# Kernel optimization log

Measured on AMD Instinct MI355X. Metric: run time of the kernel, lower is better.

Reference implementation:

```python
import jax, jax.numpy as jnp
import numpy as np
from math import sqrt

DIM = 1024
RANK = 64
B, T = 4, 4096

def _xavier(key, shape):
    fan_in, fan_out = shape[1], shape[0]
    limit = sqrt(6.0 / (fan_in + fan_out))
    return jax.random.uniform(key, shape, jnp.float32, -limit, limit)

def setup_inputs() -> dict:
    key = jax.random.key(0)
    kx, kq, kk, kv = jax.random.split(key, 4)
    return {
        "x": jax.random.normal(kx, (B, T, DIM), jnp.float32),
        "Q": _xavier(kq, (RANK, DIM)),
        "K": _xavier(kk, (RANK, DIM)),
        "VO": _xavier(kv, (DIM, DIM)),
    }

def reference(x, Q, K, VO):
    dim = x.shape[-1]
    # low-rank projections: [b, t, r]
    xq = jnp.einsum('btd,rd->btr', x, Q)
    xk = jnp.einsum('bue,re->bur', x, K)
    scores = jnp.einsum('btr,bur->btu', xq, xk) / sqrt(dim)
    attn = jax.nn.softmax(scores, axis=2)
    # attn @ x @ VO: contract with VO first (cheap [b,u,d]@[d,e]) then attn
    return jnp.einsum('btu,bue->bte', attn, x @ VO)
```

## Files before the change

kernel.cpp:

```cpp
#include <hip/hip_runtime.h>
#include <hip/hip_bf16.h>

#define BATCH 4
#define SEQ   4096
#define DIM   1024
#define RANK  64

typedef __attribute__((ext_vector_type(8))) short short8;
typedef __attribute__((ext_vector_type(4))) short short4v;
typedef __attribute__((ext_vector_type(4))) float f32x4;

#define MFMA16(a,b,c) __builtin_amdgcn_mfma_f32_16x16x32_bf16((a),(b),(c),0,0,0)

#define XQ_OFF 0
#define XK_OFF (BATCH*SEQ*RANK)
#define VT_OFF (2*BATCH*SEQ*RANK)
#define VT_END (VT_OFF + BATCH*DIM*SEQ)
#define P_OFF  ((size_t)VT_END)
#define P_LEN  ((size_t)BATCH*SEQ*SEQ)

__device__ __forceinline__ short f2b(float f) {
    __hip_bfloat16 h = __float2bfloat16(f);
    short s; __builtin_memcpy(&s, &h, sizeof(short));
    return s;
}
__device__ __forceinline__ float b2f(short s) {
    __hip_bfloat16 h; __builtin_memcpy(&h, &s, sizeof(short));
    return __bfloat162float(h);
}
__device__ __forceinline__ short8 cvt8(const float* __restrict__ p) {
    const float4 f0 = *reinterpret_cast<const float4*>(p);
    const float4 f1 = *reinterpret_cast<const float4*>(p + 4);
    short8 r;
    r[0]=f2b(f0.x); r[1]=f2b(f0.y); r[2]=f2b(f0.z); r[3]=f2b(f0.w);
    r[4]=f2b(f1.x); r[5]=f2b(f1.y); r[6]=f2b(f1.z); r[7]=f2b(f1.w);
    return r;
}
__device__ __forceinline__ void gld16(const short* g, short* l) {
    __builtin_amdgcn_global_load_lds(
        (const __attribute__((address_space(1))) void*)g,
        (__attribute__((address_space(3))) void*)l, 16, 0, 0);
}

__global__ __launch_bounds__(256) void lr_cvt(const float* __restrict__ x,
                                              const float* __restrict__ VO,
                                              const float* __restrict__ Qw,
                                              const float* __restrict__ Kw,
                                              short* __restrict__ xb,
                                              short* __restrict__ VOt,
                                              short* __restrict__ Wb)
{
    const int bid = blockIdx.x, tid = threadIdx.x;
    if (bid < 8192) {
        const size_t base = ((size_t)bid*256 + tid)*8;
        *reinterpret_cast<short8*>(xb + base) = cvt8(x + base);
    } else if (bid < 8448) {
        __shared__ short tr[64*68];
        const int bb = bid - 8192;
        const int dt = bb >> 4, et = bb & 15;
        const int d0 = dt*64, e0 = et*64;
        const int ein = tid & 63, din = tid >> 6;
        #pragma unroll
        for (int j = 0; j < 16; ++j) {
            const int dl = din + j*4;
            tr[ein*68 + dl] = f2b(VO[(size_t)(d0 + dl)*DIM + e0 + ein]);
        }
        __syncthreads();
        const int or_ = tid >> 4, oc = (tid & 15)*4;
        #pragma unroll
        for (int j = 0; j < 4; ++j) {
            const int el = or_ + j*16;
            short4v v;
            v[0]=tr[el*68+oc]; v[1]=tr[el*68+oc+1];
            v[2]=tr[el*68+oc+2]; v[3]=tr[el*68+oc+3];
            *reinterpret_cast<short4v*>(VOt + (size_t)(e0+el)*DIM + d0 + oc) = v;
        }
    } else {
        const int gid = (bid - 8448)*256 + tid;
        const int row = gid >> 7, c8 = (gid & 127)*8;
        const float* src = (row < 64 ? Qw + (size_t)row*DIM
                                     : Kw + (size_t)(row-64)*DIM) + c8;
        *reinterpret_cast<short8*>(Wb + (size_t)row*DIM + c8) = cvt8(src);
    }
}

__global__ __launch_bounds__(256, 4) void lr_proj2(const short* __restrict__ xb,
                                                   const short* __restrict__ Wb,
                                                   short* __restrict__ ws)
{
    __shared__ __align__(16) short As[128*64];
    __shared__ __align__(16) short Bs[128*64];
    const int t0 = blockIdx.x*128;
    const int tid = threadIdx.x, lane = tid & 63, w = tid >> 6;
    const int l15 = lane & 15, g = lane >> 4;
    const int wr = w >> 1, wc = w & 1;
    const short* Ab = xb + (size_t)t0*DIM;
    const short* Bb = Wb;
    const int srow = lane >> 3;
    const int skc  = ((lane & 7) ^ srow)*8;
    const int rx = l15 & 7;

    f32x4 acc[4][4] = {};
    #pragma unroll
    for (int j = 0; j < 4; ++j) {
        const int ch = 4*w + j, row = ch*8 + srow;
        gld16(Ab + (size_t)row*DIM + skc, &As[ch*512]);
        gld16(Bb + (size_t)row*DIM + skc, &Bs[ch*512]);
    }
    for (int kt = 0; kt < 16; ++kt) {
        __syncthreads();
        #pragma unroll
        for (int ks = 0; ks < 2; ++ks) {
            short8 af[4], bfr[4];
            #pragma unroll
            for (int mr = 0; mr < 4; ++mr)
                af[mr] = *reinterpret_cast<const short8*>(
                    &As[(wr*64 + mr*16 + l15)*64 + ((ks*4 + g) ^ rx)*8]);
            #pragma unroll
            for (int ct = 0; ct < 4; ++ct)
                bfr[ct] = *reinterpret_cast<const short8*>(
                    &Bs[(wc*64 + ct*16 + l15)*64 + ((ks*4 + g) ^ rx)*8]);
            #pragma unroll
            for (int mr = 0; mr < 4; ++mr)
                #pragma unroll
                for (int ct = 0; ct < 4; ++ct)
                    acc[mr][ct] = MFMA16(af[mr], bfr[ct], acc[mr][ct]);
        }
        if (kt < 15) {
            __syncthreads();
            const int k0 = (kt + 1)*64;
            #pragma unroll
            for (int j = 0; j < 4; ++j) {
                const int ch = 4*w + j, row = ch*8 + srow;
                gld16(Ab + (size_t)row*DIM + k0 + skc, &As[ch*512]);
                gld16(Bb + (size_t)row*DIM + k0 + skc, &Bs[ch*512]);
            }
        }
    }
    short* xqp = ws + XQ_OFF;
    short* xkp = ws + XK_OFF;
    #pragma unroll
    for (int mr = 0; mr < 4; ++mr)
        #pragma unroll
        for (int rr = 0; rr < 4; ++rr) {
            const int t = t0 + wr*64 + mr*16 + g*4 + rr;
            #pragma unroll
            for (int ct = 0; ct < 4; ++ct) {
                const int r = wc*64 + ct*16 + l15;
                const short v = f2b(acc[mr][ct][rr]);
                if (r < RANK) xqp[(size_t)t*RANK + r] = v;
                else          xkp[(size_t)t*RANK + r - RANK] = v;
            }
        }
}

__global__ __launch_bounds__(512, 2) void lr_vg8(const short* __restrict__ VOt,
                                                 const short* __restrict__ xb,
                                                 short* __restrict__ vT)
{
    extern __shared__ __align__(16) short lds[];
    short* As = lds;
    short* Bs = lds + 32768;
    const int bid = blockIdx.x;
    const int xcd = bid & 7, jb = bid >> 3;
    const int et = xcd >> 1;
    const int bu = (xcd & 1)*32 + jb;
    const int b = bu >> 4, ut = bu & 15;
    const int e0 = et*256, u0 = ut*256;
    const int tid = threadIdx.x, lane = tid & 63, w = tid >> 6;
    const int wr = w >> 2, wc = w & 3;
    const int l15 = lane & 15, g = lane >> 4;
    const int rx = l15 & 7;

    const short* Ab = VOt + (size_t)e0*DIM;
    const short* Bb = xb + ((size_t)(b*SEQ) + u0)*DIM;

    int aA0[2], aA1[2], aB0[2], aB1[2];
    int dA0[2], dA1[2], dB0[2], dB1[2];
    #pragma unroll
    for (int j = 0; j < 2; ++j) {
        const int s = tid + 512*j;
        const int cl = s >> 6, v = s & 63;
        const int vr = v >> 3, vk = ((v & 7) ^ vr)*8;
        const int cA0 = (cl < 8) ? cl : cl + 8;
        const int cA1 = cA0 + 8;
        const int cB0 = ((cl >> 2) << 3) + (cl & 3);
        const int cB1 = cB0 + 4;
        aA0[j] = (cA0*8 + vr)*DIM + vk;  dA0[j] = cA0*512 + v*8;
        aA1[j] = (cA1*8 + vr)*DIM + vk;  dA1[j] = cA1*512 + v*8;
        aB0[j] = (cB0*8 + vr)*DIM + vk;  dB0[j] = cB0*512 + v*8;
        aB1[j] = (cB1*8 + vr)*DIM + vk;  dB1[j] = cB1*512 + v*8;
    }

    f32x4 acc[8][4] = {};
    short8 af[4][2], bf[4][2];

    #pragma unroll
    for (int j = 0; j < 2; ++j) gld16(Ab + aA0[j], &As[dA0[j]]);
    #pragma unroll
    for (int j = 0; j < 2; ++j) gld16(Bb + aB0[j], &Bs[dB0[j]]);
    #pragma unroll
    for (int j = 0; j < 2; ++j) gld16(Bb + aB1[j], &Bs[dB1[j]]);
    #pragma unroll
    for (int j = 0; j < 2; ++j) gld16(Ab + aA1[j], &As[dA1[j]]);
    asm volatile("s_waitcnt vmcnt(4)" ::: "memory");
    __builtin_amdgcn_s_barrier();
    __builtin_amdgcn_sched_barrier(0);

    for (int kt = 0; kt < 15; ++kt) {
        const int buf  = (kt & 1) ? 16384 : 0;
        const int nbuf = 16384 - buf;
        const int kn = (kt + 1)*64;
        const int arow = buf + (wr*128 + l15)*64;
        const int brow = buf + (wc*64 + l15)*64;
        #pragma unroll
        for (int mf = 0; mf < 4; ++mf)
            #pragma unroll
            for (int ks = 0; ks < 2; ++ks)
                af[mf][ks] = *reinterpret_cast<const short8*>(
                    &As[arow + mf*1024 + ((ks*4 + g) ^ rx)*8]);
        #pragma unroll
        for (int nf = 0; nf < 2; ++nf)
            #pragma unroll
            for (int ks = 0; ks < 2; ++ks)
                bf[nf][ks] = *reinterpret_cast<const short8*>(
                    &Bs[brow + nf*1024 + ((ks*4 + g) ^ rx)*8]);
        #pragma unroll
        for (int j = 0; j < 2; ++j) gld16(Ab + aA0[j] + kn, &As[nbuf + dA0[j]]);
        __builtin_amdgcn_s_barrier();
        asm volatile("s_waitcnt lgkmcnt(0)" ::: "memory");
        __builtin_amdgcn_sched_barrier(0);
        __builtin_amdgcn_s_setprio(1);
        #pragma unroll
        for (int mf = 0; mf < 4; ++mf)
            #pragma unroll
            for (int nf = 0; nf < 2; ++nf)
                #pragma unroll
                for (int ks = 0; ks < 2; ++ks)
                    acc[mf][nf] = MFMA16(af[mf][ks], bf[nf][ks], acc[mf][nf]);
        __builtin_amdgcn_s_setprio(0);
        asm volatile("s_waitcnt vmcnt(4)" ::: "memory");
        __builtin_amdgcn_s_barrier();
        __builtin_amdgcn_sched_barrier(0);
        #pragma unroll
        for (int nf = 2; nf < 4; ++nf)
            #pragma unroll
            for (int ks = 0; ks < 2; ++ks)
                bf[nf][ks] = *reinterpret_cast<const short8*>(
                    &Bs[brow + nf*1024 + ((ks*4 + g) ^ rx)*8]);
        #pragma unroll
        for (int j = 0; j < 2; ++j) gld16(Bb + aB0[j] + kn, &Bs[nbuf + dB0[j]]);
        __builtin_amdgcn_s_barrier();
        asm volatile("s_waitcnt lgkmcnt(0)" ::: "memory");
        __builtin_amdgcn_sched_barrier(0);
        __builtin_amdgcn_s_setprio(1);
        #pragma unroll
        for (int mf = 0; mf < 4; ++mf)
            #pragma unroll
            for (int nf = 2; nf < 4; ++nf)
                #pragma unroll
                for (int ks = 0; ks < 2; ++ks)
                    acc[mf][nf] = MFMA16(af[mf][ks], bf[nf][ks], acc[mf][nf]);
        __builtin_amdgcn_s_setprio(0);
        asm volatile("s_waitcnt vmcnt(4)" ::: "memory");
        __builtin_amdgcn_s_barrier();
        __builtin_amdgcn_sched_barrier(0);
        #pragma unroll
        for (int mf = 0; mf < 4; ++mf)
            #pragma unroll
            for (int ks = 0; ks < 2; ++ks)
                af[mf][ks] = *reinterpret_cast<const short8*>(
                    &As[arow + 4096 + mf*1024 + ((ks*4 + g) ^ rx)*8]);
        #pragma unroll
        for (int j = 0; j < 2; ++j) gld16(Bb + aB1[j] + kn, &Bs[nbuf + dB1[j]]);
        __builtin_amdgcn_s_barrier();
        asm volatile("s_waitcnt lgkmcnt(0)" ::: "memory");
        __builtin_amdgcn_sched_barrier(0);
        __builtin_amdgcn_s_setprio(1);
        #pragma unroll
        for (int mf = 0; mf < 4; ++mf)
            #pragma unroll
            for (int nf = 0; nf < 2; ++nf)
                #pragma unroll
                for (int ks = 0; ks < 2; ++ks)
                    acc[mf+4][nf] = MFMA16(af[mf][ks], bf[nf][ks], acc[mf+4][nf]);
        __builtin_amdgcn_s_setprio(0);
        __builtin_amdgcn_s_barrier();
        __builtin_amdgcn_sched_barrier(0);
        #pragma unroll
        for (int j = 0; j < 2; ++j) gld16(Ab + aA1[j] + kn, &As[nbuf + dA1[j]]);
        __builtin_amdgcn_s_setprio(1);
        #pragma unroll
        for (int mf = 0; mf < 4; ++mf)
            #pragma unroll
            for (int nf = 2; nf < 4; ++nf)
                #pragma unroll
                for (int ks = 0; ks < 2; ++ks)
                    acc[mf+4][nf] = MFMA16(af[mf][ks], bf[nf][ks], acc[mf+4][nf]);
        __builtin_amdgcn_s_setprio(0);
        asm volatile("s_waitcnt vmcnt(4)" ::: "memory");
        __builtin_amdgcn_s_barrier();
        __builtin_amdgcn_sched_barrier(0);
    }
    asm volatile("s_waitcnt vmcnt(0)" ::: "memory");
    __builtin_amdgcn_s_barrier();
    __builtin_amdgcn_sched_barrier(0);
    {
        const int arow = 16384 + (wr*128 + l15)*64;
        const int brow = 16384 + (wc*64 + l15)*64;
        #pragma unroll
        for (int mf = 0; mf < 4; ++mf)
            #pragma unroll
            for (int ks = 0; ks < 2; ++ks)
                af[mf][ks] = *reinterpret_cast<const short8*>(
                    &As[arow + mf*1024 + ((ks*4 + g) ^ rx)*8]);
        #pragma unroll
        for (int nf = 0; nf < 4; ++nf)
            #pragma unroll
            for (int ks = 0; ks < 2; ++ks)
                bf[nf][ks] = *reinterpret_cast<const short8*>(
                    &Bs[brow + nf*1024 + ((ks*4 + g) ^ rx)*8]);
        #pragma unroll
        for (int mf = 0; mf < 4; ++mf)
            #pragma unroll
            for (int nf = 0; nf < 4; ++nf)
                #pragma unroll
                for (int ks = 0; ks < 2; ++ks)
                    acc[mf][nf] = MFMA16(af[mf][ks], bf[nf][ks], acc[mf][nf]);
        #pragma unroll
        for (int mf = 0; mf < 4; ++mf)
            #pragma unroll
            for (int ks = 0; ks < 2; ++ks)
                af[mf][ks] = *reinterpret_cast<const short8*>(
                    &As[arow + 4096 + mf*1024 + ((ks*4 + g) ^ rx)*8]);
        #pragma unroll
        for (int mf = 0; mf < 4; ++mf)
            #pragma unroll
            for (int nf = 0; nf < 4; ++nf)
                #pragma unroll
                for (int ks = 0; ks < 2; ++ks)
                    acc[mf+4][nf] = MFMA16(af[mf][ks], bf[nf][ks], acc[mf+4][nf]);
    }
    #pragma unroll
    for (int mf = 0; mf < 8; ++mf)
        #pragma unroll
        for (int rr = 0; rr < 4; ++rr) {
            const int e = e0 + wr*128 + mf*16 + g*4 + rr;
            short* orow = vT + ((size_t)(b*DIM) + e)*SEQ + u0 + wc*64;
            #pragma unroll
            for (int nf = 0; nf < 4; ++nf)
                orow[nf*16 + l15] = f2b(acc[mf][nf][rr]);
        }
}

__global__ __launch_bounds__(256, 4) void lr_vgemm2(const short* __restrict__ VOt,
                                                    const short* __restrict__ xb,
                                                    short* __restrict__ vT)
{
    __shared__ __align__(16) short As[128*64];
    __shared__ __align__(16) short Bs[128*64];
    const int i = blockIdx.x;
    const int etile = i & 7, j = i >> 3;
    const int ut = j & 31, b = j >> 5;
    const int e0 = etile*128, u0 = ut*128;
    const int tid = threadIdx.x, lane = tid & 63, w = tid >> 6;
    const int l15 = lane & 15, g = lane >> 4;
    const int wr = w >> 1, wc = w & 1;
    const short* Ab = VOt + (size_t)e0*DIM;
    const short* Bb = xb + ((size_t)(b*SEQ) + u0)*DIM;
    const int srow = lane >> 3;
    const int skc  = ((lane & 7) ^ srow)*8;
    const int rx = l15 & 7;

    f32x4 acc[4][4] = {};
    #pragma unroll
    for (int jj = 0; jj < 4; ++jj) {
        const int ch = 4*w + jj, row = ch*8 + srow;
        gld16(Ab + (size_t)row*DIM + skc, &As[ch*512]);
        gld16(Bb + (size_t)row*DIM + skc, &Bs[ch*512]);
    }
    for (int kt = 0; kt < 16; ++kt) {
        __syncthreads();
        #pragma unroll
        for (int ks = 0; ks < 2; ++ks) {
            short8 af[4], bfr[4];
            #pragma unroll
            for (int mr = 0; mr < 4; ++mr)
                af[mr] = *reinterpret_cast<const short8*>(
                    &As[(wr*64 + mr*16 + l15)*64 + ((ks*4 + g) ^ rx)*8]);
            #pragma unroll
            for (int ct = 0; ct < 4; ++ct)
                bfr[ct] = *reinterpret_cast<const short8*>(
                    &Bs[(wc*64 + ct*16 + l15)*64 + ((ks*4 + g) ^ rx)*8]);
            #pragma unroll
            for (int mr = 0; mr < 4; ++mr)
                #pragma unroll
                for (int ct = 0; ct < 4; ++ct)
                    acc[mr][ct] = MFMA16(af[mr], bfr[ct], acc[mr][ct]);
        }
        if (kt < 15) {
            __syncthreads();
            const int k0 = (kt + 1)*64;
            #pragma unroll
            for (int jj = 0; jj < 4; ++jj) {
                const int ch = 4*w + jj, row = ch*8 + srow;
                gld16(Ab + (size_t)row*DIM + k0 + skc, &As[ch*512]);
                gld16(Bb + (size_t)row*DIM + k0 + skc, &Bs[ch*512]);
            }
        }
    }
    #pragma unroll
    for (int mr = 0; mr < 4; ++mr)
        #pragma unroll
        for (int rr = 0; rr < 4; ++rr) {
            const int e = e0 + wr*64 + mr*16 + g*4 + rr;
            short* orow = vT + ((size_t)(b*DIM) + e)*SEQ + u0 + wc*64;
            #pragma unroll
            for (int ct = 0; ct < 4; ++ct)
                orow[ct*16 + l15] = f2b(acc[mr][ct][rr]);
        }
}

__global__ __launch_bounds__(256, 4) void lr_pexp(const short* __restrict__ ws,
                                                  short* __restrict__ P,
                                                  float* __restrict__ ps)
{
    __shared__ __align__(16) short ptile[128*136];
    __shared__ float sred[4][128];
    const int i = blockIdx.x;
    const int qt = i >> 5, ut = i & 31;
    const int b = qt >> 5;
    const int tid = threadIdx.x, lane = tid & 63, w = tid >> 6;
    const int l15 = lane & 15, g = lane >> 4;
    const float cl = 0.045084220f;
    const int q0 = qt*128;

    const short* xqb = ws + XQ_OFF + (size_t)q0*RANK;
    const short* xkb = ws + XK_OFF + ((size_t)(b*SEQ) + ut*128)*RANK;

    f32x4 acc[2][8] = {};
    #pragma unroll
    for (int ks = 0; ks < 2; ++ks) {
        short8 ak[2], bq[8];
        #pragma unroll
        for (int mr = 0; mr < 2; ++mr)
            ak[mr] = *reinterpret_cast<const short8*>(
                xkb + (size_t)(32*w + mr*16 + l15)*RANK + ks*32 + g*8);
        #pragma unroll
        for (int ct = 0; ct < 8; ++ct)
            bq[ct] = *reinterpret_cast<const short8*>(
                xqb + (size_t)(ct*16 + l15)*RANK + ks*32 + g*8);
        #pragma unroll
        for (int mr = 0; mr < 2; ++mr)
            #pragma unroll
            for (int ct = 0; ct < 8; ++ct)
                acc[mr][ct] = MFMA16(ak[mr], bq[ct], acc[mr][ct]);
    }
    float s[8] = {0.f,0.f,0.f,0.f,0.f,0.f,0.f,0.f};
    #pragma unroll
    for (int mr = 0; mr < 2; ++mr)
        #pragma unroll
        for (int ct = 0; ct < 8; ++ct) {
            short4v pk;
            #pragma unroll
            for (int r = 0; r < 4; ++r) {
                const short pb = f2b(__builtin_amdgcn_exp2f(acc[mr][ct][r]*cl));
                pk[r] = pb;
                s[ct] += b2f(pb);
            }
            *reinterpret_cast<short4v*>(
                &ptile[(ct*16 + l15)*136 + 32*w + mr*16 + g*4]) = pk;
        }
    #pragma unroll
    for (int ct = 0; ct < 8; ++ct) {
        s[ct] += __shfl_xor(s[ct], 16);
        s[ct] += __shfl_xor(s[ct], 32);
    }
    if (g == 0) {
        #pragma unroll
        for (int ct = 0; ct < 8; ++ct) sred[w][ct*16 + l15] = s[ct];
    }
    __syncthreads();
    #pragma unroll
    for (int j = 0; j < 8; ++j) {
        const int id = tid + 256*j;
        const int row = id >> 4, seg = id & 15;
        const uint4 v = *reinterpret_cast<const uint4*>(&ptile[row*136 + seg*8]);
        *reinterpret_cast<uint4*>(
            P + (size_t)(q0 + row)*SEQ + ut*128 + seg*8) = v;
    }
    if (tid < 128)
        ps[(size_t)(q0 + tid)*32 + ut] =
            sred[0][tid] + sred[1][tid] + sred[2][tid] + sred[3][tid];
}

__global__ __launch_bounds__(256) void lr_psum(const float* __restrict__ ps,
                                               float* __restrict__ linv)
{
    const int gq = blockIdx.x*256 + threadIdx.x;
    const float* p = ps + (size_t)gq*32;
    float s = 0.f;
    #pragma unroll
    for (int j = 0; j < 32; ++j) s += p[j];
    linv[gq] = 1.0f / s;
}

__global__ __launch_bounds__(512, 2) void lr_pv8(const short* __restrict__ P,
                                                 const short* __restrict__ vT,
                                                 const float* __restrict__ ps,
                                                 float* __restrict__ out)
{
    extern __shared__ __align__(16) short lds[];
    __shared__ float linv_lds[256];
    short* As = lds;
    short* Bs = lds + 32768;
    const int bid = blockIdx.x;
    const int qt = (bid & 7)*8 + (bid >> 5);
    const int nt = (bid >> 3) & 3;
    const int q0 = qt*256, d0 = nt*256, b = qt >> 4;
    const int tid = threadIdx.x, lane = tid & 63, w = tid >> 6;
    const int wr = w >> 2, wc = w & 3;
    const int l15 = lane & 15, g = lane >> 4;
    const int rx = l15 & 7;

    if (tid < 256) {
        const float* pp = ps + (size_t)(q0 + tid)*32;
        float s = 0.f;
        #pragma unroll
        for (int jj = 0; jj < 32; ++jj) s += pp[jj];
        linv_lds[tid] = 1.0f / s;
    }
    asm volatile("s_waitcnt vmcnt(0)" ::: "memory");
    __builtin_amdgcn_sched_barrier(0);

    const short* Ab = P + (size_t)q0*SEQ;
    const short* Bb = vT + ((size_t)(b*DIM) + d0)*SEQ;

    int aA0[2], aA1[2], aB0[2], aB1[2];
    int dA0[2], dA1[2], dB0[2], dB1[2];
    #pragma unroll
    for (int j = 0; j < 2; ++j) {
        const int s = tid + 512*j;
        const int cl = s >> 6, v = s & 63;
        const int vr = v >> 3, vk = ((v & 7) ^ vr)*8;
        const int cA0 = (cl < 8) ? cl : cl + 8;
        const int cA1 = cA0 + 8;
        const int cB0 = ((cl >> 2) << 3) + (cl & 3);
        const int cB1 = cB0 + 4;
        aA0[j] = (cA0*8 + vr)*SEQ + vk;  dA0[j] = cA0*512 + v*8;
        aA1[j] = (cA1*8 + vr)*SEQ + vk;  dA1[j] = cA1*512 + v*8;
        aB0[j] = (cB0*8 + vr)*SEQ + vk;  dB0[j] = cB0*512 + v*8;
        aB1[j] = (cB1*8 + vr)*SEQ + vk;  dB1[j] = cB1*512 + v*8;
    }

    f32x4 acc[8][4] = {};
    short8 af[4][2], bf[4][2];

    #pragma unroll
    for (int j = 0; j < 2; ++j) gld16(Ab + aA0[j], &As[dA0[j]]);
    #pragma unroll
    for (int j = 0; j < 2; ++j) gld16(Bb + aB0[j], &Bs[dB0[j]]);
    #pragma unroll
    for (int j = 0; j < 2; ++j) gld16(Bb + aB1[j], &Bs[dB1[j]]);
    #pragma unroll
    for (int j = 0; j < 2; ++j) gld16(Ab + aA1[j], &As[dA1[j]]);
    asm volatile("s_waitcnt vmcnt(4)" ::: "memory");
    __builtin_amdgcn_s_barrier();
    __builtin_amdgcn_sched_barrier(0);

    for (int kt = 0; kt < 63; ++kt) {
        const int buf  = (kt & 1) ? 16384 : 0;
        const int nbuf = 16384 - buf;
        const int kn = (kt + 1)*64;
        const int arow = buf + (wr*128 + l15)*64;
        const int brow = buf + (wc*64 + l15)*64;
        #pragma unroll
        for (int mf = 0; mf < 4; ++mf)
            #pragma unroll
            for (int ks = 0; ks < 2; ++ks)
                af[mf][ks] = *reinterpret_cast<const short8*>(
                    &As[arow + mf*1024 + ((ks*4 + g) ^ rx)*8]);
        #pragma unroll
        for (int nf = 0; nf < 2; ++nf)
            #pragma unroll
            for (int ks = 0; ks < 2; ++ks)
                bf[nf][ks] = *reinterpret_cast<const short8*>(
                    &Bs[brow + nf*1024 + ((ks*4 + g) ^ rx)*8]);
        #pragma unroll
        for (int j = 0; j < 2; ++j) gld16(Ab + aA0[j] + kn, &As[nbuf + dA0[j]]);
        __builtin_amdgcn_s_barrier();
        asm volatile("s_waitcnt lgkmcnt(0)" ::: "memory");
        __builtin_amdgcn_sched_barrier(0);
        __builtin_amdgcn_s_setprio(1);
        #pragma unroll
        for (int mf = 0; mf < 4; ++mf)
            #pragma unroll
            for (int nf = 0; nf < 2; ++nf)
                #pragma unroll
                for (int ks = 0; ks < 2; ++ks)
                    acc[mf][nf] = MFMA16(af[mf][ks], bf[nf][ks], acc[mf][nf]);
        __builtin_amdgcn_s_setprio(0);
        asm volatile("s_waitcnt vmcnt(4)" ::: "memory");
        __builtin_amdgcn_s_barrier();
        __builtin_amdgcn_sched_barrier(0);
        #pragma unroll
        for (int nf = 2; nf < 4; ++nf)
            #pragma unroll
            for (int ks = 0; ks < 2; ++ks)
                bf[nf][ks] = *reinterpret_cast<const short8*>(
                    &Bs[brow + nf*1024 + ((ks*4 + g) ^ rx)*8]);
        #pragma unroll
        for (int j = 0; j < 2; ++j) gld16(Bb + aB0[j] + kn, &Bs[nbuf + dB0[j]]);
        __builtin_amdgcn_s_barrier();
        asm volatile("s_waitcnt lgkmcnt(0)" ::: "memory");
        __builtin_amdgcn_sched_barrier(0);
        __builtin_amdgcn_s_setprio(1);
        #pragma unroll
        for (int mf = 0; mf < 4; ++mf)
            #pragma unroll
            for (int nf = 2; nf < 4; ++nf)
                #pragma unroll
                for (int ks = 0; ks < 2; ++ks)
                    acc[mf][nf] = MFMA16(af[mf][ks], bf[nf][ks], acc[mf][nf]);
        __builtin_amdgcn_s_setprio(0);
        asm volatile("s_waitcnt vmcnt(4)" ::: "memory");
        __builtin_amdgcn_s_barrier();
        __builtin_amdgcn_sched_barrier(0);
        #pragma unroll
        for (int mf = 0; mf < 4; ++mf)
            #pragma unroll
            for (int ks = 0; ks < 2; ++ks)
                af[mf][ks] = *reinterpret_cast<const short8*>(
                    &As[arow + 4096 + mf*1024 + ((ks*4 + g) ^ rx)*8]);
        #pragma unroll
        for (int j = 0; j < 2; ++j) gld16(Bb + aB1[j] + kn, &Bs[nbuf + dB1[j]]);
        __builtin_amdgcn_s_barrier();
        asm volatile("s_waitcnt lgkmcnt(0)" ::: "memory");
        __builtin_amdgcn_sched_barrier(0);
        __builtin_amdgcn_s_setprio(1);
        #pragma unroll
        for (int mf = 0; mf < 4; ++mf)
            #pragma unroll
            for (int nf = 0; nf < 2; ++nf)
                #pragma unroll
                for (int ks = 0; ks < 2; ++ks)
                    acc[mf+4][nf] = MFMA16(af[mf][ks], bf[nf][ks], acc[mf+4][nf]);
        __builtin_amdgcn_s_setprio(0);
        __builtin_amdgcn_s_barrier();
        __builtin_amdgcn_sched_barrier(0);
        #pragma unroll
        for (int j = 0; j < 2; ++j) gld16(Ab + aA1[j] + kn, &As[nbuf + dA1[j]]);
        __builtin_amdgcn_s_setprio(1);
        #pragma unroll
        for (int mf = 0; mf < 4; ++mf)
            #pragma unroll
            for (int nf = 2; nf < 4; ++nf)
                #pragma unroll
                for (int ks = 0; ks < 2; ++ks)
                    acc[mf+4][nf] = MFMA16(af[mf][ks], bf[nf][ks], acc[mf+4][nf]);
        __builtin_amdgcn_s_setprio(0);
        asm volatile("s_waitcnt vmcnt(4)" ::: "memory");
        __builtin_amdgcn_s_barrier();
        __builtin_amdgcn_sched_barrier(0);
    }
    asm volatile("s_waitcnt vmcnt(0)" ::: "memory");
    __builtin_amdgcn_s_barrier();
    __builtin_amdgcn_sched_barrier(0);
    {
        const int arow = 16384 + (wr*128 + l15)*64;
        const int brow = 16384 + (wc*64 + l15)*64;
        #pragma unroll
        for (int mf = 0; mf < 4; ++mf)
            #pragma unroll
            for (int ks = 0; ks < 2; ++ks)
                af[mf][ks] = *reinterpret_cast<const short8*>(
                    &As[arow + mf*1024 + ((ks*4 + g) ^ rx)*8]);
        #pragma unroll
        for (int nf = 0; nf < 4; ++nf)
            #pragma unroll
            for (int ks = 0; ks < 2; ++ks)
                bf[nf][ks] = *reinterpret_cast<const short8*>(
                    &Bs[brow + nf*1024 + ((ks*4 + g) ^ rx)*8]);
        #pragma unroll
        for (int mf = 0; mf < 4; ++mf)
            #pragma unroll
            for (int nf = 0; nf < 4; ++nf)
                #pragma unroll
                for (int ks = 0; ks < 2; ++ks)
                    acc[mf][nf] = MFMA16(af[mf][ks], bf[nf][ks], acc[mf][nf]);
        #pragma unroll
        for (int mf = 0; mf < 4; ++mf)
            #pragma unroll
            for (int ks = 0; ks < 2; ++ks)
                af[mf][ks] = *reinterpret_cast<const short8*>(
                    &As[arow + 4096 + mf*1024 + ((ks*4 + g) ^ rx)*8]);
        #pragma unroll
        for (int mf = 0; mf < 4; ++mf)
            #pragma unroll
            for (int nf = 0; nf < 4; ++nf)
                #pragma unroll
                for (int ks = 0; ks < 2; ++ks)
                    acc[mf+4][nf] = MFMA16(af[mf][ks], bf[nf][ks], acc[mf+4][nf]);
    }
    #pragma unroll
    for (int mf = 0; mf < 8; ++mf)
        #pragma unroll
        for (int rr = 0; rr < 4; ++rr) {
            const int ql = wr*128 + mf*16 + g*4 + rr;
            const float sc = linv_lds[ql];
            float* rp = out + (size_t)(q0 + ql)*DIM + d0 + wc*64;
            #pragma unroll
            for (int nf = 0; nf < 4; ++nf)
                rp[nf*16 + l15] = acc[mf][nf][rr]*sc;
        }
}

__global__ __launch_bounds__(256, 4) void lr_pv(const short* __restrict__ P,
                                                const short* __restrict__ vT,
                                                const float* __restrict__ linv,
                                                float* __restrict__ out)
{
    __shared__ __align__(16) short As[128*64];
    __shared__ __align__(16) short Bs[128*64];
    const int i = blockIdx.x;
    const int qlo = i & 7, j = i >> 3;
    const int nt = j & 7, qhi = j >> 3;
    const int qt = qhi*8 + qlo;
    const int q0 = qt*128, d0 = nt*128, b = qt >> 5;
    const int tid = threadIdx.x, lane = tid & 63, w = tid >> 6;
    const int l15 = lane & 15, g = lane >> 4;
    const int wr = w >> 1, wc = w & 1;

    const short* Ab = P + (size_t)q0*SEQ;
    const short* Bb = vT + ((size_t)(b*DIM) + d0)*SEQ;
    const int srow = lane >> 3;
    const int skc  = ((lane & 7) ^ srow)*8;
    const int rx = l15 & 7;

    f32x4 acc[4][4] = {};
    #pragma unroll
    for (int jj = 0; jj < 4; ++jj) {
        const int ch = 4*w + jj, row = ch*8 + srow;
        gld16(Ab + (size_t)row*SEQ + skc, &As[ch*512]);
        gld16(Bb + (size_t)row*SEQ + skc, &Bs[ch*512]);
    }
    for (int kt = 0; kt < 64; ++kt) {
        __syncthreads();
        #pragma unroll
        for (int ks = 0; ks < 2; ++ks) {
            short8 af[4], bfr[4];
            #pragma unroll
            for (int mr = 0; mr < 4; ++mr)
                af[mr] = *reinterpret_cast<const short8*>(
                    &As[(wr*64 + mr*16 + l15)*64 + ((ks*4 + g) ^ rx)*8]);
            #pragma unroll
            for (int ct = 0; ct < 4; ++ct)
                bfr[ct] = *reinterpret_cast<const short8*>(
                    &Bs[(wc*64 + ct*16 + l15)*64 + ((ks*4 + g) ^ rx)*8]);
            #pragma unroll
            for (int mr = 0; mr < 4; ++mr)
                #pragma unroll
                for (int ct = 0; ct < 4; ++ct)
                    acc[mr][ct] = MFMA16(af[mr], bfr[ct], acc[mr][ct]);
        }
        if (kt < 63) {
            __syncthreads();
            const int k0 = (kt + 1)*64;
            #pragma unroll
            for (int jj = 0; jj < 4; ++jj) {
                const int ch = 4*w + jj, row = ch*8 + srow;
                gld16(Ab + (size_t)row*SEQ + k0 + skc, &As[ch*512]);
                gld16(Bb + (size_t)row*SEQ + k0 + skc, &Bs[ch*512]);
            }
        }
    }
    #pragma unroll
    for (int mr = 0; mr < 4; ++mr)
        #pragma unroll
        for (int rr = 0; rr < 4; ++rr) {
            const int q = q0 + wr*64 + mr*16 + g*4 + rr;
            const float sc = linv[q];
            float* rp = out + (size_t)q*DIM + d0 + wc*64;
            #pragma unroll
            for (int ct = 0; ct < 4; ++ct)
                rp[ct*16 + l15] = acc[mr][ct][rr]*sc;
        }
}

__global__ __launch_bounds__(256) void lr_proj(const float* __restrict__ x,
                                               const float* __restrict__ Qw,
                                               const float* __restrict__ Kw,
                                               short* __restrict__ ws)
{
    __shared__ __align__(16) short ldsB[64*40];
    const int i = blockIdx.x;
    const int ttile = i & 63, b = i >> 6;
    const int tid = threadIdx.x, lane = tid & 63, w = tid >> 6;
    const int l15 = lane & 15, g = lane >> 4;
    const int t0 = ttile * 64;

    f32x4 acc[2][4] = {};
    for (int e0 = 0; e0 < DIM; e0 += 32) {
        const int tr = tid >> 2, seg = tid & 3;
        const float* px = x + (size_t)(b*SEQ + t0 + tr)*DIM + e0 + seg*8;
        const float4 f0 = *reinterpret_cast<const float4*>(px);
        const float4 f1 = *reinterpret_cast<const float4*>(px + 4);
        __syncthreads();
        {
            short* d = &ldsB[tr*40 + seg*8];
            d[0]=f2b(f0.x); d[1]=f2b(f0.y); d[2]=f2b(f0.z); d[3]=f2b(f0.w);
            d[4]=f2b(f1.x); d[5]=f2b(f1.y); d[6]=f2b(f1.z); d[7]=f2b(f1.w);
        }
        __syncthreads();
        #pragma unroll
        for (int mr = 0; mr < 2; ++mr) {
            const int r = 32*w + mr*16 + l15;
            const float* wp = (r < RANK ? Qw + (size_t)r*DIM
                                        : Kw + (size_t)(r - RANK)*DIM) + e0 + g*8;
            const short8 a = cvt8(wp);
            #pragma unroll
            for (int ct = 0; ct < 4; ++ct) {
                const short8 bb = *reinterpret_cast<const short8*>(
                    &ldsB[(ct*16 + l15)*40 + g*8]);
                acc[mr][ct] = MFMA16(a, bb, acc[mr][ct]);
            }
        }
    }
    short* xqp = ws + XQ_OFF;
    short* xkp = ws + XK_OFF;
    #pragma unroll
    for (int mr = 0; mr < 2; ++mr) {
        const int rb = 32*w + mr*16 + g*4;
        short* base = (rb < RANK) ? (xqp + rb) : (xkp + (rb - RANK));
        #pragma unroll
        for (int ct = 0; ct < 4; ++ct) {
            const int t = t0 + ct*16 + l15;
            short4v pk;
            pk[0]=f2b(acc[mr][ct][0]); pk[1]=f2b(acc[mr][ct][1]);
            pk[2]=f2b(acc[mr][ct][2]); pk[3]=f2b(acc[mr][ct][3]);
            *reinterpret_cast<short4v*>(base + (size_t)(b*SEQ + t)*RANK) = pk;
        }
    }
}

__global__ __launch_bounds__(256) void lr_vgemm(const float* __restrict__ x,
                                                const float* __restrict__ VO,
                                                short* __restrict__ ws)
{
    short* vT = ws + VT_OFF;
    __shared__ __align__(16) short ldsA[128*40];
    __shared__ __align__(16) short ldsB[128*40];
    const int i = blockIdx.x;
    const int dtile = i & 7, utile = (i >> 3) & 31, b = i >> 8;
    const int d0 = dtile*128, u0 = utile*128;
    const int tid = threadIdx.x, lane = tid & 63, w = tid >> 6;
    const int l15 = lane & 15, g = lane >> 4;
    const int wr = w >> 1, wc = w & 1;

    f32x4 acc[4][4] = {};
    for (int e0 = 0; e0 < DIM; e0 += 32) {
        const int dcol = tid & 127, erg = (tid >> 7)*16;
        float va[16];
        #pragma unroll
        for (int j = 0; j < 16; ++j)
            va[j] = VO[(size_t)(e0 + erg + j)*DIM + d0 + dcol];
        const int ur = tid >> 1, esg = (tid & 1)*16;
        const float* pb = x + (size_t)(b*SEQ + u0 + ur)*DIM + e0 + esg;
        float4 vb0 = reinterpret_cast<const float4*>(pb)[0];
        float4 vb1 = reinterpret_cast<const float4*>(pb)[1];
        float4 vb2 = reinterpret_cast<const float4*>(pb)[2];
        float4 vb3 = reinterpret_cast<const float4*>(pb)[3];
        __syncthreads();
        #pragma unroll
        for (int j = 0; j < 16; ++j) ldsA[dcol*40 + erg + j] = f2b(va[j]);
        {
            short* d = &ldsB[ur*40 + esg];
            d[0]=f2b(vb0.x); d[1]=f2b(vb0.y); d[2]=f2b(vb0.z); d[3]=f2b(vb0.w);
            d[4]=f2b(vb1.x); d[5]=f2b(vb1.y); d[6]=f2b(vb1.z); d[7]=f2b(vb1.w);
            d[8]=f2b(vb2.x); d[9]=f2b(vb2.y); d[10]=f2b(vb2.z); d[11]=f2b(vb2.w);
            d[12]=f2b(vb3.x); d[13]=f2b(vb3.y); d[14]=f2b(vb3.z); d[15]=f2b(vb3.w);
        }
        __syncthreads();
        short8 af[4], bfr[4];
        #pragma unroll
        for (int mr = 0; mr < 4; ++mr)
            af[mr] = *reinterpret_cast<const short8*>(
                &ldsA[(wr*64 + mr*16 + l15)*40 + g*8]);
        #pragma unroll
        for (int ct = 0; ct < 4; ++ct)
            bfr[ct] = *reinterpret_cast<const short8*>(
                &ldsB[(wc*64 + ct*16 + l15)*40 + g*8]);
        #pragma unroll
        for (int mr = 0; mr < 4; ++mr)
            #pragma unroll
            for (int ct = 0; ct < 4; ++ct)
                acc[mr][ct] = MFMA16(af[mr], bfr[ct], acc[mr][ct]);
    }
    #pragma unroll
    for (int mr = 0; mr < 4; ++mr)
        #pragma unroll
        for (int rr = 0; rr < 4; ++rr) {
            const int d = d0 + wr*64 + mr*16 + g*4 + rr;
            short* orow = vT + (size_t)(b*DIM + d)*SEQ + u0 + wc*64;
            #pragma unroll
            for (int ct = 0; ct < 4; ++ct)
                orow[ct*16 + l15] = f2b(acc[mr][ct][rr]);
        }
}

__global__ __launch_bounds__(256) void lr_stats(const short* __restrict__ ws,
                                                float* __restrict__ pm,
                                                float* __restrict__ pl)
{
    const short* xq = ws + XQ_OFF;
    const short* xk = ws + XK_OFF;
    const int i = blockIdx.x;
    const int us = i & 3, qtile = (i >> 2) & 63, b = i >> 8;
    const int tid = threadIdx.x, lane = tid & 63, w = tid >> 6;
    const int l15 = lane & 15, g = lane >> 4;
    const float cl = 0.045084220f;

    short8 qb0, qb1;
    {
        const short* p = xq + (size_t)(b*SEQ + qtile*64 + 16*w + l15)*RANK + g*8;
        qb0 = *reinterpret_cast<const short8*>(p);
        qb1 = *reinterpret_cast<const short8*>(p + 32);
    }
    const short* kb = xk + (size_t)b*SEQ*RANK;

    float m = -3.0e38f, l = 0.f;
    for (int it = 0; it < 16; ++it) {
        const int ub = us*1024 + it*64;
        f32x4 S[4];
        #pragma unroll
        for (int t = 0; t < 4; ++t) {
            const short* kp = kb + (size_t)(ub + 16*t + l15)*RANK + g*8;
            const short8 a0 = *reinterpret_cast<const short8*>(kp);
            const short8 a1 = *reinterpret_cast<const short8*>(kp + 32);
            f32x4 z = {};
            z = MFMA16(a0, qb0, z);
            z = MFMA16(a1, qb1, z);
            S[t] = z;
        }
        float mt = S[0][0];
        #pragma unroll
        for (int t = 0; t < 4; ++t)
            #pragma unroll
            for (int r = 0; r < 4; ++r) mt = fmaxf(mt, S[t][r]);
        const float mn = fmaxf(m, mt);
        l *= __builtin_amdgcn_exp2f((m - mn)*cl);
        const float mc = mn*cl;
        #pragma unroll
        for (int t = 0; t < 4; ++t)
            #pragma unroll
            for (int r = 0; r < 4; ++r)
                l += __builtin_amdgcn_exp2f(__builtin_fmaf(S[t][r], cl, -mc));
        m = mn;
    }
    #pragma unroll
    for (int mask = 16; mask <= 32; mask <<= 1) {
        const float mo = __shfl_xor(m, mask), lo = __shfl_xor(l, mask);
        const float mn = fmaxf(m, mo);
        l = l*__builtin_amdgcn_exp2f((m - mn)*cl)
          + lo*__builtin_amdgcn_exp2f((mo - mn)*cl);
        m = mn;
    }
    if (g == 0) {
        const int idx = (b*SEQ + qtile*64 + 16*w + l15)*4 + us;
        pm[idx] = m; pl[idx] = l;
    }
}

__global__ __launch_bounds__(256, 4) void lr_flash(const short* __restrict__ ws,
                                                   const float* __restrict__ pm,
                                                   const float* __restrict__ pl,
                                                   float* __restrict__ out)
{
    const short* xq = ws + XQ_OFF;
    const short* xk = ws + XK_OFF;
    const short* vT = ws + VT_OFF;
    __shared__ __align__(16) short vlds[128*64];
    __shared__ __align__(16) short plds[32*64];
    const int i = blockIdx.x;
    const int xcd = i & 7, slot = i >> 3;
    const int combo = xcd + 8*(slot >> 6);
    const int qtile = slot & 63;
    const int b = combo >> 2, dch = combo & 3;
    const int tid = threadIdx.x, lane = tid & 63, w = tid >> 6;
    const int l15 = lane & 15, g = lane >> 4;
    const float cl = 0.045084220f;

    float mC;
    {
        const int base = (b*SEQ + qtile*64 + 16*w + l15)*4;
        const float m0 = pm[base+0], m1 = pm[base+1];
        const float m2 = pm[base+2], m3 = pm[base+3];
        const float mm = fmaxf(fmaxf(m0, m1), fmaxf(m2, m3));
        const float l = pl[base+0]*__builtin_amdgcn_exp2f((m0-mm)*cl)
                      + pl[base+1]*__builtin_amdgcn_exp2f((m1-mm)*cl)
                      + pl[base+2]*__builtin_amdgcn_exp2f((m2-mm)*cl)
                      + pl[base+3]*__builtin_amdgcn_exp2f((m3-mm)*cl);
        mC = -(mm*cl + __builtin_amdgcn_logf(l));
    }
    short8 qb0, qb1;
    {
        const short* p = xq + (size_t)(b*SEQ + qtile*64 + 16*w + l15)*RANK + g*8;
        qb0 = *reinterpret_cast<const short8*>(p);
        qb1 = *reinterpret_cast<const short8*>(p + 32);
    }
    const short* vbase = vT + ((size_t)b*DIM + dch*256)*SEQ;
    const short* kr = xk + (size_t)b*SEQ*RANK + l15*RANK + g*8;
    const int r7 = l15 >> 1;
    const int st_dst = (tid >> 3)*64 + (((tid & 7) ^ ((tid >> 3) & 7))*8);
    const int st_src = (tid >> 2)*SEQ + (tid & 3)*8;
    const int a_base = r7*64 + ((((l15 & 1)*4 + g) ^ r7)*8);
    const int b_base = (32*w + r7)*64 + ((((l15 & 1)*4 + g) ^ r7)*8);
    const int chv = (l15 & 1)*4 + (g >> 1);
    const int pw0 = (8*w + r7)*64 + ((chv ^ r7)*8)       + (g & 1)*4;
    const int pw1 = (8*w + r7)*64 + (((chv + 2) ^ r7)*8) + (g & 1)*4;

    uint4 sreg[4];
    #pragma unroll
    for (int c = 0; c < 4; ++c)
        sreg[c] = *reinterpret_cast<const uint4*>(vbase + st_src + (size_t)c*64*SEQ);
    #pragma unroll
    for (int c = 0; c < 4; ++c)
        *reinterpret_cast<uint4*>(&vlds[st_dst + 2048*c]) = sreg[c];

    f32x4 O[16] = {};
    for (int ub = 0; ub < SEQ; ub += 32) {
        const bool more = (ub + 32 < SEQ);
        if (more) {
            #pragma unroll
            for (int c = 0; c < 4; ++c)
                sreg[c] = *reinterpret_cast<const uint4*>(
                    vbase + st_src + ub + 32 + (size_t)c*64*SEQ);
        }
        #pragma unroll
        for (int t = 0; t < 2; ++t) {
            const short* kp = kr + (size_t)(ub + 16*t)*RANK;
            const short8 a0 = *reinterpret_cast<const short8*>(kp);
            const short8 a1 = *reinterpret_cast<const short8*>(kp + 32);
            f32x4 z = {};
            z = MFMA16(a0, qb0, z);
            z = MFMA16(a1, qb1, z);
            short4v pk;
            #pragma unroll
            for (int r = 0; r < 4; ++r)
                pk[r] = f2b(__builtin_amdgcn_exp2f(__builtin_fmaf(z[r], cl, mC)));
            *reinterpret_cast<short4v*>(&plds[t ? pw1 : pw0]) = pk;
        }
        __syncthreads();
        short8 pa[4];
        #pragma unroll
        for (int qt = 0; qt < 4; ++qt)
            pa[qt] = *reinterpret_cast<const short8*>(&plds[a_base + qt*512]);
        #pragma unroll
        for (int dt = 0; dt < 4; ++dt) {
            const short8 vf = *reinterpret_cast<const short8*>(&vlds[b_base + dt*512]);
            #pragma unroll
            for (int qt = 0; qt < 4; ++qt)
                O[qt*4 + dt] = MFMA16(pa[qt], vf, O[qt*4 + dt]);
        }
        __syncthreads();
        if (more) {
            #pragma unroll
            for (int c = 0; c < 4; ++c)
                *reinterpret_cast<uint4*>(&vlds[st_dst + 2048*c]) = sreg[c];
        }
    }
    #pragma unroll
    for (int qt = 0; qt < 4; ++qt)
        #pragma unroll
        for (int rr = 0; rr < 4; ++rr) {
            const int q = qtile*64 + qt*16 + g*4 + rr;
            float* rowp = out + (size_t)(b*SEQ + q)*DIM + dch*256 + 64*w;
            #pragma unroll
            for (int dt = 0; dt < 4; ++dt)
                rowp[dt*16 + l15] = O[qt*4 + dt][rr];
        }
}

extern "C" void kernel_launch(void* const* d_in, const int* in_sizes, int n_in,
                              void* d_out, int out_size, void* d_ws, size_t ws_size,
                              hipStream_t stream) {
    const float* x  = (const float*)d_in[0];
    const float* Q  = (const float*)d_in[1];
    const float* K  = (const float*)d_in[2];
    const float* VO = (const float*)d_in[3];
    float* out = (float*)d_out;
    short* ws = (short*)d_ws;

    const size_t need = (P_OFF + P_LEN)*2 + (size_t)(BATCH*SEQ)*(32 + 1)*4;
    if (ws_size >= need) {
        short* Pb  = ws + P_OFF;
        short* xb  = Pb;
        short* VOt = Pb + (size_t)BATCH*SEQ*DIM;
        short* Wb  = VOt + (size_t)DIM*DIM;
        float* ps  = (float*)(ws + P_OFF + P_LEN);
        float* linv = ps + (size_t)BATCH*SEQ*32;
        const hipError_t e1 = hipFuncSetAttribute(
            reinterpret_cast<const void*>(lr_pv8),
            hipFuncAttributeMaxDynamicSharedMemorySize, 131072);
        const hipError_t e2 = hipFuncSetAttribute(
            reinterpret_cast<const void*>(lr_vg8),
            hipFuncAttributeMaxDynamicSharedMemorySize, 131072);
        lr_cvt   <<<dim3(8512), dim3(256), 0, stream>>>(x, VO, Q, K, xb, VOt, Wb);
        lr_proj2 <<<dim3(128),  dim3(256), 0, stream>>>(xb, Wb, ws);
        if (e2 == hipSuccess)
            lr_vg8   <<<dim3(256), dim3(512), 131072, stream>>>(VOt, xb, ws + VT_OFF);
        else
            lr_vgemm2<<<dim3(1024), dim3(256), 0, stream>>>(VOt, xb, ws + VT_OFF);
        lr_pexp  <<<dim3(4096), dim3(256), 0, stream>>>(ws, Pb, ps);
        if (e1 == hipSuccess) {
            lr_pv8<<<dim3(256), dim3(512), 131072, stream>>>(Pb, ws + VT_OFF, ps, out);
        } else {
            lr_psum<<<dim3(64), dim3(256), 0, stream>>>(ps, linv);
            lr_pv  <<<dim3(1024), dim3(256), 0, stream>>>(Pb, ws + VT_OFF, linv, out);
        }
    } else {
        float* pm = (float*)(ws + VT_END);
        float* pl = pm + BATCH*SEQ*4;
        lr_proj <<<dim3(256),  dim3(256), 0, stream>>>(x, Q, K, ws);
        lr_stats<<<dim3(1024), dim3(256), 0, stream>>>(ws, pm, pl);
        lr_vgemm<<<dim3(1024), dim3(256), 0, stream>>>(x, VO, ws);
        lr_flash<<<dim3(1024), dim3(256), 0, stream>>>(ws, pm, pl, out);
    }
}
```

Measured before the change: 235.9 us.

## Deepen PV GEMM global-to-LDS prefetch to two k-tiles ahead

The prologue now loads two k-tiles into both LDS buffers, and the main loop issues loads for tile k+2 into the buffer as soon as its subtiles are consumed. The last A1 chunk of tile k+1 is also loaded during tile k. Intermediate vmcnt waits are removed and a single vmcnt(6) wait per iteration replaces them, so more global loads are in flight while MFMAs run. The separate epilogue iteration is folded into the loop under predicates. The tradeoff is more complex buffer-reuse ordering, with a risk of races if the barriers do not fully guard overwrites of the current buffer.

```diff
diff --git a/kernel.cpp b/kernel.cpp
--- a/kernel.cpp
+++ b/kernel.cpp
@@ -557,23 +557,29 @@
     short8 af[4][2], bf[4][2];
 
     #pragma unroll
-    for (int j = 0; j < 2; ++j) gld16(Ab + aA0[j], &As[dA0[j]]);
-    #pragma unroll
-    for (int j = 0; j < 2; ++j) gld16(Bb + aB0[j], &Bs[dB0[j]]);
-    #pragma unroll
-    for (int j = 0; j < 2; ++j) gld16(Bb + aB1[j], &Bs[dB1[j]]);
-    #pragma unroll
-    for (int j = 0; j < 2; ++j) gld16(Ab + aA1[j], &As[dA1[j]]);
-    asm volatile("s_waitcnt vmcnt(4)" ::: "memory");
+    for (int t = 0; t < 2; ++t) {
+        const int bo = t ? 16384 : 0, ko = t*64;
+        #pragma unroll
+        for (int j = 0; j < 2; ++j) gld16(Ab + aA0[j] + ko, &As[bo + dA0[j]]);
+        #pragma unroll
+        for (int j = 0; j < 2; ++j) gld16(Bb + aB0[j] + ko, &Bs[bo + dB0[j]]);
+        #pragma unroll
+        for (int j = 0; j < 2; ++j) gld16(Bb + aB1[j] + ko, &Bs[bo + dB1[j]]);
+        #pragma unroll
+        for (int j = 0; j < 2; ++j) gld16(Ab + aA1[j] + ko, &As[bo + dA1[j]]);
+    }
+    asm volatile("s_waitcnt vmcnt(0)" ::: "memory");
     __builtin_amdgcn_s_barrier();
     __builtin_amdgcn_sched_barrier(0);
 
-    for (int kt = 0; kt < 63; ++kt) {
+    for (int kt = 0; kt < 64; ++kt) {
         const int buf  = (kt & 1) ? 16384 : 0;
         const int nbuf = 16384 - buf;
-        const int kn = (kt + 1)*64;
+        const int k1 = (kt + 1)*64, k2 = (kt + 2)*64;
         const int arow = buf + (wr*128 + l15)*64;
         const int brow = buf + (wc*64 + l15)*64;
+        const bool st1 = (kt >= 1) && (kt < 63);
+        const bool st2 = kt < 62;
         #pragma unroll
         for (int mf = 0; mf < 4; ++mf)
             #pragma unroll
@@ -586,8 +592,11 @@
             for (int ks = 0; ks < 2; ++ks)
                 bf[nf][ks] = *reinterpret_cast<const short8*>(
                     &Bs[brow + nf*1024 + ((ks*4 + g) ^ rx)*8]);
-        #pragma unroll
-        for (int j = 0; j < 2; ++j) gld16(Ab + aA0[j] + kn, &As[nbuf + dA0[j]]);
+        if (st1) {
+            #pragma unroll
+            for (int j = 0; j < 2; ++j)
+                gld16(Ab + aA1[j] + k1, &As[nbuf + dA1[j]]);
+        }
         __builtin_amdgcn_s_barrier();
         asm volatile("s_waitcnt lgkmcnt(0)" ::: "memory");
         __builtin_amdgcn_sched_barrier(0);
@@ -600,7 +609,6 @@
                 for (int ks = 0; ks < 2; ++ks)
                     acc[mf][nf] = MFMA16(af[mf][ks], bf[nf][ks], acc[mf][nf]);
         __builtin_amdgcn_s_setprio(0);
-        asm volatile("s_waitcnt vmcnt(4)" ::: "memory");
         __builtin_amdgcn_s_barrier();
         __builtin_amdgcn_sched_barrier(0);
         #pragma unroll
@@ -609,8 +617,11 @@
             for (int ks = 0; ks < 2; ++ks)
                 bf[nf][ks] = *reinterpret_cast<const short8*>(
                     &Bs[brow + nf*1024 + ((ks*4 + g) ^ rx)*8]);
-        #pragma unroll
-        for (int j = 0; j < 2; ++j) gld16(Bb + aB0[j] + kn, &Bs[nbuf + dB0[j]]);
+        if (st2) {
+            #pragma unroll
+            for (int j = 0; j < 2; ++j)
+                gld16(Ab + aA0[j] + k2, &As[buf + dA0[j]]);
+        }
         __builtin_amdgcn_s_barrier();
         asm volatile("s_waitcnt lgkmcnt(0)" ::: "memory");
         __builtin_amdgcn_sched_barrier(0);
@@ -623,7 +634,6 @@
                 for (int ks = 0; ks < 2; ++ks)
                     acc[mf][nf] = MFMA16(af[mf][ks], bf[nf][ks], acc[mf][nf]);
         __builtin_amdgcn_s_setprio(0);
-        asm volatile("s_waitcnt vmcnt(4)" ::: "memory");
         __builtin_amdgcn_s_barrier();
         __builtin_amdgcn_sched_barrier(0);
         #pragma unroll
@@ -632,8 +642,11 @@
             for (int ks = 0; ks < 2; ++ks)
                 af[mf][ks] = *reinterpret_cast<const short8*>(
                     &As[arow + 4096 + mf*1024 + ((ks*4 + g) ^ rx)*8]);
-        #pragma unroll
-        for (int j = 0; j < 2; ++j) gld16(Bb + aB1[j] + kn, &Bs[nbuf + dB1[j]]);
+        if (st2) {
+            #pragma unroll
+            for (int j = 0; j < 2; ++j)
+                gld16(Bb + aB0[j] + k2, &Bs[buf + dB0[j]]);
+        }
         __builtin_amdgcn_s_barrier();
         asm volatile("s_waitcnt lgkmcnt(0)" ::: "memory");
         __builtin_amdgcn_sched_barrier(0);
@@ -648,8 +661,11 @@
         __builtin_amdgcn_s_setprio(0);
         __builtin_amdgcn_s_barrier();
         __builtin_amdgcn_sched_barrier(0);
-        #pragma unroll
-        for (int j = 0; j < 2; ++j) gld16(Ab + aA1[j] + kn, &As[nbuf + dA1[j]]);
+        if (st2) {
+            #pragma unroll
+            for (int j = 0; j < 2; ++j)
+                gld16(Bb + aB1[j] + k2, &Bs[buf + dB1[j]]);
+        }
         __builtin_amdgcn_s_setprio(1);
         #pragma unroll
         for (int mf = 0; mf < 4; ++mf)
@@ -659,48 +675,13 @@
                 for (int ks = 0; ks < 2; ++ks)
                     acc[mf+4][nf] = MFMA16(af[mf][ks], bf[nf][ks], acc[mf+4][nf]);
         __builtin_amdgcn_s_setprio(0);
-        asm volatile("s_waitcnt vmcnt(4)" ::: "memory");
-        __builtin_amdgcn_s_barrier();
-        __builtin_amdgcn_sched_barrier(0);
-    }
-    asm volatile("s_waitcnt vmcnt(0)" ::: "memory");
-    __builtin_amdgcn_s_barrier();
-    __builtin_amdgcn_sched_barrier(0);
-    {
-        const int arow = 16384 + (wr*128 + l15)*64;
-        const int brow = 16384 + (wc*64 + l15)*64;
-        #pragma unroll
-        for (int mf = 0; mf < 4; ++mf)
-            #pragma unroll
-            for (int ks = 0; ks < 2; ++ks)
-                af[mf][ks] = *reinterpret_cast<const short8*>(
-                    &As[arow + mf*1024 + ((ks*4 + g) ^ rx)*8]);
-        #pragma unroll
-        for (int nf = 0; nf < 4; ++nf)
-            #pragma unroll
-            for (int ks = 0; ks < 2; ++ks)
-                bf[nf][ks] = *reinterpret_cast<const short8*>(
-                    &Bs[brow + nf*1024 + ((ks*4 + g) ^ rx)*8]);
-        #pragma unroll
-        for (int mf = 0; mf < 4; ++mf)
-            #pragma unroll
-            for (int nf = 0; nf < 4; ++nf)
-                #pragma unroll
-                for (int ks = 0; ks < 2; ++ks)
-                    acc[mf][nf] = MFMA16(af[mf][ks], bf[nf][ks], acc[mf][nf]);
-        #pragma unroll
-        for (int mf = 0; mf < 4; ++mf)
-            #pragma unroll
-            for (int ks = 0; ks < 2; ++ks)
-                af[mf][ks] = *reinterpret_cast<const short8*>(
-                    &As[arow + 4096 + mf*1024 + ((ks*4 + g) ^ rx)*8]);
-        #pragma unroll
-        for (int mf = 0; mf < 4; ++mf)
-            #pragma unroll
-            for (int nf = 0; nf < 4; ++nf)
-                #pragma unroll
-                for (int ks = 0; ks < 2; ++ks)
-                    acc[mf+4][nf] = MFMA16(af[mf][ks], bf[nf][ks], acc[mf+4][nf]);
+        if (kt < 62) {
+            asm volatile("s_waitcnt vmcnt(6)" ::: "memory");
+        } else if (kt == 62) {
+            asm volatile("s_waitcnt vmcnt(0)" ::: "memory");
+        }
+        __builtin_amdgcn_s_barrier();
+        __builtin_amdgcn_sched_barrier(0);
     }
     #pragma unroll
     for (int mf = 0; mf < 8; ++mf)
```

Result: slower. 243.7 us (+3.3%).
